# Performance work log

Hardware: AMD Instinct MI355X
Metric: run time of the kernel (lower is better)

The kernel has to match this reference:

```python
import jax, jax.numpy as jnp
import numpy as np

N_NODES = 40000

def setup_inputs() -> dict:
    key = jax.random.key(0)
    k1, k2, k3, k4 = jax.random.split(key, 4)
    x = jax.random.normal(k1, (N_NODES, 256), dtype=jnp.float32)
    edge_index = jax.random.randint(k2, (2, 640000), 0, N_NODES, dtype=jnp.int64)
    W = jax.random.normal(k3, (256, 128), dtype=jnp.float32) * (1.0 / np.sqrt(256))
    b = jax.random.normal(k4, (128,), dtype=jnp.float32) * 0.01
    return {"x": x, "edge_index": edge_index, "W": W, "b": b}

def reference(x, edge_index, W, b):
    N = x.shape[0]
    # GCNConv: add self-loops, symmetric degree normalization, linear, aggregate, bias
    loops = jnp.arange(N, dtype=edge_index.dtype)
    src = jnp.concatenate([edge_index[0], loops])  # message sources j
    dst = jnp.concatenate([edge_index[1], loops])  # targets i
    ones = jnp.ones_like(dst, dtype=x.dtype)
    deg = jax.ops.segment_sum(ones, dst, num_segments=N)  # in-degree incl. self-loop
    dinv = jnp.where(deg > 0, jax.lax.rsqrt(deg), 0.0)
    norm = dinv[src] * dinv[dst]  # [E+N]
    xw = x @ W  # transform first (in_dim -> out_dim), as in PyG GCNConv
    msgs = norm[:, None] * xw[src]  # [E+N, out_dim]
    agg = jax.ops.segment_sum(msgs, dst, num_segments=N) + b
    return jax.nn.relu(agg)  # dropout_value == 0 -> no dropout
```

## Files before the change

### kernel.cpp

```cpp
#include <hip/hip_runtime.h>

#define N_NODES 40000
#define IN_DIM 256
#define OUT_DIM 128
#define CAP 64
#define GEMM_BLOCKS 625
#define FILL_BLOCKS 625

typedef __bf16 bf16x8 __attribute__((ext_vector_type(8)));
typedef float floatx4 __attribute__((ext_vector_type(4)));

__device__ __forceinline__ int clamp_idx(int v) {
    unsigned u = (unsigned)v;
    return (u < (unsigned)N_NODES) ? v : 0;
}

__device__ __forceinline__ int ld_edge(const int* e32, long long idx, int is64) {
    return is64 ? e32[2 * idx] : e32[idx];
}

__device__ __forceinline__ float bflo(unsigned u) {
    union { unsigned i; float f; } c; c.i = u << 16; return c.f;
}
__device__ __forceinline__ float bfhi(unsigned u) {
    union { unsigned i; float f; } c; c.i = u & 0xFFFF0000u; return c.f;
}

__global__ void prep_r16(const int* __restrict__ edge32, int* __restrict__ flag,
                         int* __restrict__ cnt, const float* __restrict__ W,
                         __bf16* __restrict__ wswz) {
    int i = blockIdx.x * 256 + threadIdx.x;
    if (i < N_NODES) cnt[i] = 0;
    if (i < IN_DIM * OUT_DIM) {
        int j    = i & 7;
        int lane = (i >> 3) & 63;
        int tile = i >> 9;
        int ct = tile & 7, kc = tile >> 3;
        int k = kc * 32 + (lane >> 4) * 8 + j;
        int n = ct * 16 + (lane & 15);
        wswz[i] = (__bf16)W[k * OUT_DIM + n];
    }
    if (blockIdx.x == 0) {
        __shared__ int sh[256];
        int t = threadIdx.x;
        int nz = 0;
        for (int k = t; k < 1000; k += 256) nz |= (edge32[2 * k + 1] != 0);
        sh[t] = nz;
        __syncthreads();
        for (int off = 128; off > 0; off >>= 1) {
            if (t < off) sh[t] |= sh[t + off];
            __syncthreads();
        }
        if (t == 0) *flag = sh[0] ? 0 : 1;
    }
}

__global__ __launch_bounds__(256) void gemm_r16(
    const float* __restrict__ x, const __bf16* __restrict__ wswz,
    __bf16* __restrict__ xwb) {
    int t = threadIdx.x;
    int wave = t >> 6, lane = t & 63;
    int quad = lane >> 4, m16 = lane & 15;
    int m = blockIdx.x * 64 + wave * 16 + m16;
    const float* xrow = x + (long long)m * IN_DIM;
    const bf16x8* wp = (const bf16x8*)wswz;

    floatx4 acc[8];
#pragma unroll
    for (int ct = 0; ct < 8; ++ct) acc[ct] = (floatx4){0.f, 0.f, 0.f, 0.f};

#pragma unroll
    for (int kc = 0; kc < 8; ++kc) {
        int k0 = kc * 32 + quad * 8;
        float4 xa = *(const float4*)(xrow + k0);
        float4 xb = *(const float4*)(xrow + k0 + 4);
        bf16x8 af;
        af[0] = (__bf16)xa.x; af[1] = (__bf16)xa.y;
        af[2] = (__bf16)xa.z; af[3] = (__bf16)xa.w;
        af[4] = (__bf16)xb.x; af[5] = (__bf16)xb.y;
        af[6] = (__bf16)xb.z; af[7] = (__bf16)xb.w;
#pragma unroll
        for (int ct = 0; ct < 8; ++ct) {
            bf16x8 bf = wp[(kc * 8 + ct) * 64 + lane];
            acc[ct] = __builtin_amdgcn_mfma_f32_16x16x32_bf16(af, bf, acc[ct], 0, 0, 0);
        }
    }

    unsigned* xwu = (unsigned*)xwb;
    int rbase = blockIdx.x * 64 + wave * 16 + quad * 4;
#pragma unroll
    for (int p = 0; p < 4; ++p) {
#pragma unroll
        for (int r = 0; r < 4; ++r) {
            __bf16 lo = (__bf16)acc[2 * p][r];
            __bf16 hi = (__bf16)acc[2 * p + 1][r];
            unsigned u = ((unsigned)__builtin_bit_cast(unsigned short, hi) << 16)
                       | (unsigned)__builtin_bit_cast(unsigned short, lo);
            xwu[(long long)(rbase + r) * 64 + p * 16 + m16] = u;
        }
    }
}

__global__ __launch_bounds__(256) void fill_r16(
    const void* __restrict__ edge, int E, const int* __restrict__ flag,
    int* __restrict__ cnt, unsigned short* __restrict__ bucket) {
    int is64 = *flag;
    const int* e32 = (const int*)edge;
    long long base = (long long)blockIdx.x * 1024 + threadIdx.x * 4;
    int s0 = clamp_idx(ld_edge(e32, base + 0, is64));
    int s1 = clamp_idx(ld_edge(e32, base + 1, is64));
    int s2 = clamp_idx(ld_edge(e32, base + 2, is64));
    int s3 = clamp_idx(ld_edge(e32, base + 3, is64));
    int d0 = clamp_idx(ld_edge(e32, E + base + 0, is64));
    int d1 = clamp_idx(ld_edge(e32, E + base + 1, is64));
    int d2 = clamp_idx(ld_edge(e32, E + base + 2, is64));
    int d3 = clamp_idx(ld_edge(e32, E + base + 3, is64));
    int p0 = atomicAdd(&cnt[d0], 1);
    int p1 = atomicAdd(&cnt[d1], 1);
    int p2 = atomicAdd(&cnt[d2], 1);
    int p3 = atomicAdd(&cnt[d3], 1);
    if (p0 < CAP) bucket[d0 * CAP + p0] = (unsigned short)s0;
    if (p1 < CAP) bucket[d1 * CAP + p1] = (unsigned short)s1;
    if (p2 < CAP) bucket[d2 * CAP + p2] = (unsigned short)s2;
    if (p3 < CAP) bucket[d3 * CAP + p3] = (unsigned short)s3;
}

__global__ void gather_r16(const unsigned short* __restrict__ bucket,
                           const int* __restrict__ cnt,
                           const unsigned* __restrict__ xwd, const float* __restrict__ b,
                           float* __restrict__ out) {
    int node = blockIdx.x * 4 + (threadIdx.x >> 6);
    int lane = threadIdx.x & 63;
    if (node >= N_NODES) return;
    int cc = (lane >> 4) * 32 + (lane & 15);
    float b0 = b[cc], b1 = b[cc + 16];
    int cn_true = cnt[node];
    int take = cn_true < CAP ? cn_true : CAP;
    float dd = rsqrtf((float)(cn_true + 1));
    unsigned us = xwd[node * 64 + lane];
    float a0 = dd * dd * bflo(us);
    float a1 = dd * dd * bfhi(us);

    int s_l = 0; float nrm_l = 0.0f;
    if (lane < take) {
        s_l = (int)bucket[node * CAP + lane];
        nrm_l = dd * rsqrtf((float)(cnt[s_l] + 1));
    }
    int j = 0;
    for (; j + 8 <= take; j += 8) {
        int   s0 = __shfl(s_l, j),     s1 = __shfl(s_l, j + 1);
        int   s2 = __shfl(s_l, j + 2), s3 = __shfl(s_l, j + 3);
        int   s4 = __shfl(s_l, j + 4), s5 = __shfl(s_l, j + 5);
        int   s6 = __shfl(s_l, j + 6), s7 = __shfl(s_l, j + 7);
        float n0 = __shfl(nrm_l, j),     n1 = __shfl(nrm_l, j + 1);
        float n2 = __shfl(nrm_l, j + 2), n3 = __shfl(nrm_l, j + 3);
        float n4 = __shfl(nrm_l, j + 4), n5 = __shfl(nrm_l, j + 5);
        float n6 = __shfl(nrm_l, j + 6), n7 = __shfl(nrm_l, j + 7);
        unsigned u0 = xwd[s0 * 64 + lane], u1 = xwd[s1 * 64 + lane];
        unsigned u2 = xwd[s2 * 64 + lane], u3 = xwd[s3 * 64 + lane];
        unsigned u4 = xwd[s4 * 64 + lane], u5 = xwd[s5 * 64 + lane];
        unsigned u6 = xwd[s6 * 64 + lane], u7 = xwd[s7 * 64 + lane];
        a0 += n0 * bflo(u0); a1 += n0 * bfhi(u0);
        a0 += n1 * bflo(u1); a1 += n1 * bfhi(u1);
        a0 += n2 * bflo(u2); a1 += n2 * bfhi(u2);
        a0 += n3 * bflo(u3); a1 += n3 * bfhi(u3);
        a0 += n4 * bflo(u4); a1 += n4 * bfhi(u4);
        a0 += n5 * bflo(u5); a1 += n5 * bfhi(u5);
        a0 += n6 * bflo(u6); a1 += n6 * bfhi(u6);
        a0 += n7 * bflo(u7); a1 += n7 * bfhi(u7);
    }
    for (; j < take; ++j) {
        int   s = __shfl(s_l, j);
        float n = __shfl(nrm_l, j);
        unsigned u = xwd[s * 64 + lane];
        a0 += n * bflo(u); a1 += n * bfhi(u);
    }
    out[(long long)node * OUT_DIM + cc]      = fmaxf(a0 + b0, 0.0f);
    out[(long long)node * OUT_DIM + cc + 16] = fmaxf(a1 + b1, 0.0f);
}

extern "C" void kernel_launch(void* const* d_in, const int* in_sizes, int n_in,
                              void* d_out, int out_size, void* d_ws, size_t ws_size,
                              hipStream_t stream) {
    const float* x   = (const float*)d_in[0];
    const void* edge = d_in[1];
    const float* W   = (const float*)d_in[2];
    const float* b   = (const float*)d_in[3];
    float* out       = (float*)d_out;

    int E = in_sizes[1] / 2;

    char* ws = (char*)d_ws;
    int*            cnt    = (int*)(ws);
    int*            flag   = (int*)(ws + 160000);
    __bf16*         wswz   = (__bf16*)(ws + 160256);
    unsigned short* bucket = (unsigned short*)(ws + 225792);
    __bf16*         xwb    = (__bf16*)(ws + 5345792);

    prep_r16<<<160, 256, 0, stream>>>((const int*)edge, flag, cnt, W, wswz);
    fill_r16<<<FILL_BLOCKS, 256, 0, stream>>>(edge, E, flag, cnt, bucket);
    gemm_r16<<<GEMM_BLOCKS, 256, 0, stream>>>(x, wswz, xwb);
    gather_r16<<<N_NODES / 4, 256, 0, stream>>>(bucket, cnt, (const unsigned*)xwb, b, out);
}
```

Measured before the change: 160.3 us.

## Merge GEMM and bucket-fill into one launch, add nontemporal memory hints and prefetch

```diff
diff --git a/kernel.cpp b/kernel.cpp
--- a/kernel.cpp
+++ b/kernel.cpp
@@ -15,8 +15,9 @@
     return (u < (unsigned)N_NODES) ? v : 0;
 }
 
-__device__ __forceinline__ int ld_edge(const int* e32, long long idx, int is64) {
-    return is64 ? e32[2 * idx] : e32[idx];
+__device__ __forceinline__ int ld_edge_nt(const int* e32, long long idx, int is64) {
+    return is64 ? __builtin_nontemporal_load(&e32[2 * idx])
+                : __builtin_nontemporal_load(&e32[idx]);
 }
 
 __device__ __forceinline__ float bflo(unsigned u) {
@@ -26,7 +27,7 @@
     union { unsigned i; float f; } c; c.i = u & 0xFFFF0000u; return c.f;
 }
 
-__global__ void prep_r16(const int* __restrict__ edge32, int* __restrict__ flag,
+__global__ void prep_r17(const int* __restrict__ edge32, int* __restrict__ flag,
                          int* __restrict__ cnt, const float* __restrict__ W,
                          __bf16* __restrict__ wswz) {
     int i = blockIdx.x * 256 + threadIdx.x;
@@ -55,77 +56,88 @@
     }
 }
 
-__global__ __launch_bounds__(256) void gemm_r16(
+__global__ __launch_bounds__(256) void main_r17(
     const float* __restrict__ x, const __bf16* __restrict__ wswz,
-    __bf16* __restrict__ xwb) {
-    int t = threadIdx.x;
-    int wave = t >> 6, lane = t & 63;
-    int quad = lane >> 4, m16 = lane & 15;
-    int m = blockIdx.x * 64 + wave * 16 + m16;
-    const float* xrow = x + (long long)m * IN_DIM;
-    const bf16x8* wp = (const bf16x8*)wswz;
-
-    floatx4 acc[8];
-#pragma unroll
-    for (int ct = 0; ct < 8; ++ct) acc[ct] = (floatx4){0.f, 0.f, 0.f, 0.f};
-
-#pragma unroll
-    for (int kc = 0; kc < 8; ++kc) {
-        int k0 = kc * 32 + quad * 8;
-        float4 xa = *(const float4*)(xrow + k0);
-        float4 xb = *(const float4*)(xrow + k0 + 4);
-        bf16x8 af;
-        af[0] = (__bf16)xa.x; af[1] = (__bf16)xa.y;
-        af[2] = (__bf16)xa.z; af[3] = (__bf16)xa.w;
-        af[4] = (__bf16)xb.x; af[5] = (__bf16)xb.y;
-        af[6] = (__bf16)xb.z; af[7] = (__bf16)xb.w;
-#pragma unroll
-        for (int ct = 0; ct < 8; ++ct) {
-            bf16x8 bf = wp[(kc * 8 + ct) * 64 + lane];
-            acc[ct] = __builtin_amdgcn_mfma_f32_16x16x32_bf16(af, bf, acc[ct], 0, 0, 0);
-        }
-    }
-
-    unsigned* xwu = (unsigned*)xwb;
-    int rbase = blockIdx.x * 64 + wave * 16 + quad * 4;
-#pragma unroll
-    for (int p = 0; p < 4; ++p) {
-#pragma unroll
-        for (int r = 0; r < 4; ++r) {
-            __bf16 lo = (__bf16)acc[2 * p][r];
-            __bf16 hi = (__bf16)acc[2 * p + 1][r];
-            unsigned u = ((unsigned)__builtin_bit_cast(unsigned short, hi) << 16)
-                       | (unsigned)__builtin_bit_cast(unsigned short, lo);
-            xwu[(long long)(rbase + r) * 64 + p * 16 + m16] = u;
-        }
-    }
-}
-
-__global__ __launch_bounds__(256) void fill_r16(
+    __bf16* __restrict__ xwb,
     const void* __restrict__ edge, int E, const int* __restrict__ flag,
     int* __restrict__ cnt, unsigned short* __restrict__ bucket) {
-    int is64 = *flag;
-    const int* e32 = (const int*)edge;
-    long long base = (long long)blockIdx.x * 1024 + threadIdx.x * 4;
-    int s0 = clamp_idx(ld_edge(e32, base + 0, is64));
-    int s1 = clamp_idx(ld_edge(e32, base + 1, is64));
-    int s2 = clamp_idx(ld_edge(e32, base + 2, is64));
-    int s3 = clamp_idx(ld_edge(e32, base + 3, is64));
-    int d0 = clamp_idx(ld_edge(e32, E + base + 0, is64));
-    int d1 = clamp_idx(ld_edge(e32, E + base + 1, is64));
-    int d2 = clamp_idx(ld_edge(e32, E + base + 2, is64));
-    int d3 = clamp_idx(ld_edge(e32, E + base + 3, is64));
-    int p0 = atomicAdd(&cnt[d0], 1);
-    int p1 = atomicAdd(&cnt[d1], 1);
-    int p2 = atomicAdd(&cnt[d2], 1);
-    int p3 = atomicAdd(&cnt[d3], 1);
-    if (p0 < CAP) bucket[d0 * CAP + p0] = (unsigned short)s0;
-    if (p1 < CAP) bucket[d1 * CAP + p1] = (unsigned short)s1;
-    if (p2 < CAP) bucket[d2 * CAP + p2] = (unsigned short)s2;
-    if (p3 < CAP) bucket[d3 * CAP + p3] = (unsigned short)s3;
-}
-
-__global__ void gather_r16(const unsigned short* __restrict__ bucket,
+    int t = threadIdx.x;
+    if (blockIdx.x < GEMM_BLOCKS) {
+        int wave = t >> 6, lane = t & 63;
+        int quad = lane >> 4, m16 = lane & 15;
+        int m = blockIdx.x * 64 + wave * 16 + m16;
+        const float* xrow = x + (long long)m * IN_DIM;
+        const bf16x8* wp = (const bf16x8*)wswz;
+
+        floatx4 acc[8];
+#pragma unroll
+        for (int ct = 0; ct < 8; ++ct) acc[ct] = (floatx4){0.f, 0.f, 0.f, 0.f};
+
+        float4 xa = *(const float4*)(xrow + quad * 8);
+        float4 xb = *(const float4*)(xrow + quad * 8 + 4);
+#pragma unroll
+        for (int kc = 0; kc < 8; ++kc) {
+            float4 na, nb;
+            if (kc < 7) {
+                int k1 = (kc + 1) * 32 + quad * 8;
+                na = *(const float4*)(xrow + k1);
+                nb = *(const float4*)(xrow + k1 + 4);
+            }
+            bf16x8 af;
+            af[0] = (__bf16)xa.x; af[1] = (__bf16)xa.y;
+            af[2] = (__bf16)xa.z; af[3] = (__bf16)xa.w;
+            af[4] = (__bf16)xb.x; af[5] = (__bf16)xb.y;
+            af[6] = (__bf16)xb.z; af[7] = (__bf16)xb.w;
+#pragma unroll
+            for (int ct = 0; ct < 8; ++ct) {
+                bf16x8 bf = wp[(kc * 8 + ct) * 64 + lane];
+                acc[ct] = __builtin_amdgcn_mfma_f32_16x16x32_bf16(af, bf, acc[ct], 0, 0, 0);
+            }
+            xa = na; xb = nb;
+        }
+
+        unsigned* xwu = (unsigned*)xwb;
+        int rbase = blockIdx.x * 64 + wave * 16 + quad * 4;
+#pragma unroll
+        for (int p = 0; p < 4; ++p) {
+#pragma unroll
+            for (int r = 0; r < 4; ++r) {
+                __bf16 lo = (__bf16)acc[2 * p][r];
+                __bf16 hi = (__bf16)acc[2 * p + 1][r];
+                unsigned u = ((unsigned)__builtin_bit_cast(unsigned short, hi) << 16)
+                           | (unsigned)__builtin_bit_cast(unsigned short, lo);
+                __builtin_nontemporal_store(
+                    u, &xwu[(long long)(rbase + r) * 64 + p * 16 + m16]);
+            }
+        }
+    } else {
+        int is64 = *flag;
+        const int* e32 = (const int*)edge;
+        long long base = (long long)(blockIdx.x - GEMM_BLOCKS) * 1024 + t * 4;
+        int s0 = clamp_idx(ld_edge_nt(e32, base + 0, is64));
+        int s1 = clamp_idx(ld_edge_nt(e32, base + 1, is64));
+        int s2 = clamp_idx(ld_edge_nt(e32, base + 2, is64));
+        int s3 = clamp_idx(ld_edge_nt(e32, base + 3, is64));
+        int d0 = clamp_idx(ld_edge_nt(e32, E + base + 0, is64));
+        int d1 = clamp_idx(ld_edge_nt(e32, E + base + 1, is64));
+        int d2 = clamp_idx(ld_edge_nt(e32, E + base + 2, is64));
+        int d3 = clamp_idx(ld_edge_nt(e32, E + base + 3, is64));
+        int p0 = atomicAdd(&cnt[d0], 1);
+        int p1 = atomicAdd(&cnt[d1], 1);
+        int p2 = atomicAdd(&cnt[d2], 1);
+        int p3 = atomicAdd(&cnt[d3], 1);
+        if (p0 < CAP)
+            __builtin_nontemporal_store((unsigned short)s0, &bucket[d0 * CAP + p0]);
+        if (p1 < CAP)
+            __builtin_nontemporal_store((unsigned short)s1, &bucket[d1 * CAP + p1]);
+        if (p2 < CAP)
+            __builtin_nontemporal_store((unsigned short)s2, &bucket[d2 * CAP + p2]);
+        if (p3 < CAP)
+            __builtin_nontemporal_store((unsigned short)s3, &bucket[d3 * CAP + p3]);
+    }
+}
+
+__global__ void gather_r17(const unsigned short* __restrict__ bucket,
                            const int* __restrict__ cnt,
                            const unsigned* __restrict__ xwd, const float* __restrict__ b,
                            float* __restrict__ out) {
@@ -143,7 +155,7 @@
 
     int s_l = 0; float nrm_l = 0.0f;
     if (lane < take) {
-        s_l = (int)bucket[node * CAP + lane];
+        s_l = (int)__builtin_nontemporal_load(&bucket[node * CAP + lane]);
         nrm_l = dd * rsqrtf((float)(cnt[s_l] + 1));
     }
     int j = 0;
@@ -175,8 +187,10 @@
         unsigned u = xwd[s * 64 + lane];
         a0 += n * bflo(u); a1 += n * bfhi(u);
     }
-    out[(long long)node * OUT_DIM + cc]      = fmaxf(a0 + b0, 0.0f);
-    out[(long long)node * OUT_DIM + cc + 16] = fmaxf(a1 + b1, 0.0f);
+    __builtin_nontemporal_store(fmaxf(a0 + b0, 0.0f),
+                                &out[(long long)node * OUT_DIM + cc]);
+    __builtin_nontemporal_store(fmaxf(a1 + b1, 0.0f),
+                                &out[(long long)node * OUT_DIM + cc + 16]);
 }
 
 extern "C" void kernel_launch(void* const* d_in, const int* in_sizes, int n_in,
@@ -197,8 +211,8 @@
     unsigned short* bucket = (unsigned short*)(ws + 225792);
     __bf16*         xwb    = (__bf16*)(ws + 5345792);
 
-    prep_r16<<<160, 256, 0, stream>>>((const int*)edge, flag, cnt, W, wswz);
-    fill_r16<<<FILL_BLOCKS, 256, 0, stream>>>(edge, E, flag, cnt, bucket);
-    gemm_r16<<<GEMM_BLOCKS, 256, 0, stream>>>(x, wswz, xwb);
-    gather_r16<<<N_NODES / 4, 256, 0, stream>>>(bucket, cnt, (const unsigned*)xwb, b, out);
-}
+    prep_r17<<<160, 256, 0, stream>>>((const int*)edge, flag, cnt, W, wswz);
+    main_r17<<<GEMM_BLOCKS + FILL_BLOCKS, 256, 0, stream>>>(
+        x, wswz, xwb, edge, E, flag, cnt, bucket);
+    gather_r17<<<N_NODES / 4, 256, 0, stream>>>(bucket, cnt, (const unsigned*)xwb, b, out);
+}
```

New measurement: 168.2 us. +4.9%, slower.
